# Kernel optimization log

Hardware: AMD Instinct MI355X
Metric: run time of the kernel (lower is better)

Reference implementation:

```python
import jax, jax.numpy as jnp
import numpy as np


def setup_inputs() -> dict:
    key = jax.random.key(0)
    ks = jax.random.split(key, 4)
    B, T, I, H, O = 1024, 512, 64, 128, 10
    return {
        "x": jax.random.normal(ks[0], (B, T, I), dtype=jnp.float32),
        "W_hx": jax.random.normal(ks[1], (H, I), dtype=jnp.float32) * (6.0 / (H + I)) ** 0.5,
        "W_hh": jax.random.normal(ks[2], (H, H), dtype=jnp.float32) * (6.0 / (H + H)) ** 0.5,
        "b_hh": jnp.zeros((H,), dtype=jnp.float32),
        "W_ph": jax.random.normal(ks[3], (O, H), dtype=jnp.float32) * (6.0 / (O + H)) ** 0.5,
        "b_ph": jnp.zeros((O,), dtype=jnp.float32),
    }


def reference(x, W_hx, W_hh, b_hh, W_ph, b_ph):
    B, T, I = x.shape
    H = W_hh.shape[0]
    # Precompute input projections for all timesteps in one GEMM: [B,T,H]
    xproj = jnp.einsum("bti,hi->bth", x, W_hx)
    h0 = jnp.zeros((B, H), dtype=x.dtype)

    def step(h, xp_t):
        # xp_t: [B,H]; recurrent update h = tanh(W_hx x_t + W_hh h + b)
        h_new = jnp.tanh(xp_t + h @ W_hh.T + b_hh)
        return h_new, None

    # scan over time (leading axis): xproj transposed to [T,B,H]
    h_T, _ = jax.lax.scan(step, h0, jnp.swapaxes(xproj, 0, 1))
    return h_T @ W_ph.T + b_ph
```

## Files before the change

### kernel.cpp

```cpp
#include <hip/hip_runtime.h>
#include <math.h>


#define T_STEPS 512
#define I_DIM   64
#define H_DIM   128
#define O_DIM   10
#define BT      16
#define PITCH   136

typedef short  bf16x8 __attribute__((ext_vector_type(8)));
typedef float  f32x4  __attribute__((ext_vector_type(4)));

static __device__ inline short f2bf(float f) {
    union { float f; unsigned u; } v; v.f = f;
    unsigned r = v.u + 0x7FFFu + ((v.u >> 16) & 1u);
    return (short)(r >> 16);
}
static __device__ inline float bf2f(short s) {
    union { unsigned u; float f; } v; v.u = ((unsigned)(unsigned short)s) << 16;
    return v.f;
}

__global__ __launch_bounds__(256)
__attribute__((amdgpu_waves_per_eu(1, 2)))
void rnn_mfma_kernel(
    const float* __restrict__ x,
    const float* __restrict__ W_hx,
    const float* __restrict__ W_hh,
    const float* __restrict__ b_hh,
    const float* __restrict__ W_ph,
    const float* __restrict__ b_ph,
    float* __restrict__ out)
{
    const int b0   = blockIdx.x * BT;
    const int tid  = threadIdx.x;
    const int w    = tid >> 6;
    const int lane = tid & 63;
    const int c    = lane & 15;
    const int q    = lane >> 4;

    __shared__ short hbuf[2][BT * PITCH];

    int4 Bw[2][6];
    #pragma unroll
    for (int nt = 0; nt < 2; ++nt) {
        const int n = w * 32 + nt * 16 + c;
        #pragma unroll
        for (int kt = 0; kt < 6; ++kt) {
            const float* src = (kt < 4) ? (W_hh + n * H_DIM + kt * 32 + q * 8)
                                        : (W_hx + n * I_DIM + (kt - 4) * 32 + q * 8);
            short e[8];
            #pragma unroll
            for (int j = 0; j < 8; ++j) e[j] = f2bf(src[j]);
            Bw[nt][kt].x = ((int)(unsigned short)e[0]) | ((int)(unsigned short)e[1] << 16);
            Bw[nt][kt].y = ((int)(unsigned short)e[2]) | ((int)(unsigned short)e[3] << 16);
            Bw[nt][kt].z = ((int)(unsigned short)e[4]) | ((int)(unsigned short)e[5] << 16);
            Bw[nt][kt].w = ((int)(unsigned short)e[6]) | ((int)(unsigned short)e[7] << 16);
        }
    }
    #pragma unroll
    for (int nt = 0; nt < 2; ++nt)
        #pragma unroll
        for (int kt = 0; kt < 6; ++kt)
            asm volatile("" : "+v"(Bw[nt][kt].x), "+v"(Bw[nt][kt].y),
                              "+v"(Bw[nt][kt].z), "+v"(Bw[nt][kt].w));

    const float bias0 = b_hh[w * 32 + c];
    const float bias1 = b_hh[w * 32 + 16 + c];

    for (int idx = tid; idx < BT * PITCH; idx += 256) hbuf[0][idx] = 0;

    const float* xrow = x + (size_t)(b0 + c) * T_STEPS * I_DIM;
    float4 xr[4];
    {
        const float* p0 = xrow + 0 * I_DIM;
        xr[0] = *(const float4*)(p0 +      q * 8);
        xr[1] = *(const float4*)(p0 +      q * 8 + 4);
        xr[2] = *(const float4*)(p0 + 32 + q * 8);
        xr[3] = *(const float4*)(p0 + 32 + q * 8 + 4);
    }
    __syncthreads();

    for (int t = 0; t < T_STEPS; ++t) {
        const int p = t & 1;

        bf16x8 Ax0, Ax1;
        Ax0[0]=f2bf(xr[0].x); Ax0[1]=f2bf(xr[0].y); Ax0[2]=f2bf(xr[0].z); Ax0[3]=f2bf(xr[0].w);
        Ax0[4]=f2bf(xr[1].x); Ax0[5]=f2bf(xr[1].y); Ax0[6]=f2bf(xr[1].z); Ax0[7]=f2bf(xr[1].w);
        Ax1[0]=f2bf(xr[2].x); Ax1[1]=f2bf(xr[2].y); Ax1[2]=f2bf(xr[2].z); Ax1[3]=f2bf(xr[2].w);
        Ax1[4]=f2bf(xr[3].x); Ax1[5]=f2bf(xr[3].y); Ax1[6]=f2bf(xr[3].z); Ax1[7]=f2bf(xr[3].w);

        {
            const int tn = (t < T_STEPS - 1) ? (t + 1) : (T_STEPS - 1);
            const float* pn = xrow + (size_t)tn * I_DIM;
            xr[0] = *(const float4*)(pn +      q * 8);
            xr[1] = *(const float4*)(pn +      q * 8 + 4);
            xr[2] = *(const float4*)(pn + 32 + q * 8);
            xr[3] = *(const float4*)(pn + 32 + q * 8 + 4);
        }

        const short* hb = hbuf[p] + c * PITCH + q * 8;
        bf16x8 Ah0 = *(const bf16x8*)(hb +  0);
        bf16x8 Ah1 = *(const bf16x8*)(hb + 32);
        bf16x8 Ah2 = *(const bf16x8*)(hb + 64);
        bf16x8 Ah3 = *(const bf16x8*)(hb + 96);

        f32x4 C0 = {0.f, 0.f, 0.f, 0.f};
        f32x4 C1 = {0.f, 0.f, 0.f, 0.f};
        C0 = __builtin_amdgcn_mfma_f32_16x16x32_bf16(Ax0, __builtin_bit_cast(bf16x8, Bw[0][4]), C0, 0, 0, 0);
        C1 = __builtin_amdgcn_mfma_f32_16x16x32_bf16(Ax0, __builtin_bit_cast(bf16x8, Bw[1][4]), C1, 0, 0, 0);
        C0 = __builtin_amdgcn_mfma_f32_16x16x32_bf16(Ax1, __builtin_bit_cast(bf16x8, Bw[0][5]), C0, 0, 0, 0);
        C1 = __builtin_amdgcn_mfma_f32_16x16x32_bf16(Ax1, __builtin_bit_cast(bf16x8, Bw[1][5]), C1, 0, 0, 0);
        C0 = __builtin_amdgcn_mfma_f32_16x16x32_bf16(Ah0, __builtin_bit_cast(bf16x8, Bw[0][0]), C0, 0, 0, 0);
        C1 = __builtin_amdgcn_mfma_f32_16x16x32_bf16(Ah0, __builtin_bit_cast(bf16x8, Bw[1][0]), C1, 0, 0, 0);
        C0 = __builtin_amdgcn_mfma_f32_16x16x32_bf16(Ah1, __builtin_bit_cast(bf16x8, Bw[0][1]), C0, 0, 0, 0);
        C1 = __builtin_amdgcn_mfma_f32_16x16x32_bf16(Ah1, __builtin_bit_cast(bf16x8, Bw[1][1]), C1, 0, 0, 0);
        C0 = __builtin_amdgcn_mfma_f32_16x16x32_bf16(Ah2, __builtin_bit_cast(bf16x8, Bw[0][2]), C0, 0, 0, 0);
        C1 = __builtin_amdgcn_mfma_f32_16x16x32_bf16(Ah2, __builtin_bit_cast(bf16x8, Bw[1][2]), C1, 0, 0, 0);
        C0 = __builtin_amdgcn_mfma_f32_16x16x32_bf16(Ah3, __builtin_bit_cast(bf16x8, Bw[0][3]), C0, 0, 0, 0);
        C1 = __builtin_amdgcn_mfma_f32_16x16x32_bf16(Ah3, __builtin_bit_cast(bf16x8, Bw[1][3]), C1, 0, 0, 0);

        short* hw = hbuf[1 - p];
        #pragma unroll
        for (int r = 0; r < 4; ++r) {
            const int m = q * 4 + r;
            float s0 = C0[r] + bias0;
            float s1 = C1[r] + bias1;
            float e0 = __builtin_amdgcn_exp2f(s0 * 2.885390081777926825f);
            float e1 = __builtin_amdgcn_exp2f(s1 * 2.885390081777926825f);
            float h0 = fmaf(-2.0f, __builtin_amdgcn_rcpf(e0 + 1.0f), 1.0f);
            float h1 = fmaf(-2.0f, __builtin_amdgcn_rcpf(e1 + 1.0f), 1.0f);
            hw[m * PITCH + w * 32 + c]      = f2bf(h0);
            hw[m * PITCH + w * 32 + 16 + c] = f2bf(h1);
        }
        __syncthreads();
    }

    if (tid < BT * O_DIM) {
        const int m = tid / O_DIM;
        const int o = tid % O_DIM;
        float acc = b_ph[o];
        #pragma unroll 4
        for (int k = 0; k < H_DIM; ++k)
            acc = fmaf(W_ph[o * H_DIM + k], bf2f(hbuf[0][m * PITCH + k]), acc);
        out[(size_t)(b0 + m) * O_DIM + o] = acc;
    }
}

extern "C" void kernel_launch(void* const* d_in, const int* in_sizes, int n_in,
                              void* d_out, int out_size, void* d_ws, size_t ws_size,
                              hipStream_t stream) {
    const float* x    = (const float*)d_in[0];
    const float* W_hx = (const float*)d_in[1];
    const float* W_hh = (const float*)d_in[2];
    const float* b_hh = (const float*)d_in[3];
    const float* W_ph = (const float*)d_in[4];
    const float* b_ph = (const float*)d_in[5];
    float* out = (float*)d_out;

    rnn_mfma_kernel<<<1024 / BT, 256, 0, stream>>>(x, W_hx, W_hh, b_hh, W_ph, b_ph, out);
}
```

Measured before the change: 555.0 us.

## Unroll RNN loop by two with split accumulators and deeper x prefetch

Unrolls the time loop by two, alternating two x register buffers so x loads are prefetched two steps ahead instead of one. Each output tile is accumulated in two independent accumulator chains that are summed afterwards, which shortens the serial MFMA dependency chain. The hidden-state LDS reads now come before the x conversion, and __syncthreads is replaced with an explicit lgkmcnt wait plus s_barrier. The extra register buffers raise register pressure, and the added vector sums cost a few instructions per step.

Result: faster. 522.6 us (-5.8%).

```diff
diff --git a/kernel.cpp b/kernel.cpp
--- a/kernel.cpp
+++ b/kernel.cpp
@@ -21,6 +21,68 @@
     union { unsigned u; float f; } v; v.u = ((unsigned)(unsigned short)s) << 16;
     return v.f;
 }
+
+static __device__ inline void lds_barrier() {
+    asm volatile("s_waitcnt lgkmcnt(0)\n\ts_barrier" ::: "memory");
+}
+
+#define RNN_STEP(t, XR)                                                         \
+    {                                                                           \
+        const int p = (t) & 1;                                                  \
+         \
+        const short* hb = hbuf[p] + c * PITCH + q * 8;                          \
+        bf16x8 Ah0 = *(const bf16x8*)(hb +  0);                                 \
+        bf16x8 Ah1 = *(const bf16x8*)(hb + 32);                                 \
+        bf16x8 Ah2 = *(const bf16x8*)(hb + 64);                                 \
+        bf16x8 Ah3 = *(const bf16x8*)(hb + 96);                                 \
+          \
+          \
+        bf16x8 Ax0, Ax1;                                                        \
+        Ax0[0]=f2bf(XR[0].x); Ax0[1]=f2bf(XR[0].y); Ax0[2]=f2bf(XR[0].z); Ax0[3]=f2bf(XR[0].w); \
+        Ax0[4]=f2bf(XR[1].x); Ax0[5]=f2bf(XR[1].y); Ax0[6]=f2bf(XR[1].z); Ax0[7]=f2bf(XR[1].w); \
+        Ax1[0]=f2bf(XR[2].x); Ax1[1]=f2bf(XR[2].y); Ax1[2]=f2bf(XR[2].z); Ax1[3]=f2bf(XR[2].w); \
+        Ax1[4]=f2bf(XR[3].x); Ax1[5]=f2bf(XR[3].y); Ax1[6]=f2bf(XR[3].z); Ax1[7]=f2bf(XR[3].w); \
+        {                                                                       \
+            const int tn = ((t) + 2 < T_STEPS) ? (t) + 2 : T_STEPS - 1;         \
+            const float* pn = xrow + (size_t)tn * I_DIM;                        \
+            XR[0] = *(const float4*)(pn +      q * 8);                          \
+            XR[1] = *(const float4*)(pn +      q * 8 + 4);                      \
+            XR[2] = *(const float4*)(pn + 32 + q * 8);                          \
+            XR[3] = *(const float4*)(pn + 32 + q * 8 + 4);                      \
+        }                                                                       \
+            \
+        f32x4 C0a = {0.f,0.f,0.f,0.f}, C0b = {0.f,0.f,0.f,0.f};                 \
+        f32x4 C1a = {0.f,0.f,0.f,0.f}, C1b = {0.f,0.f,0.f,0.f};                 \
+        C0a = __builtin_amdgcn_mfma_f32_16x16x32_bf16(Ax0, __builtin_bit_cast(bf16x8, Bw[0][4]), C0a, 0, 0, 0); \
+        C1a = __builtin_amdgcn_mfma_f32_16x16x32_bf16(Ax0, __builtin_bit_cast(bf16x8, Bw[1][4]), C1a, 0, 0, 0); \
+        C0b = __builtin_amdgcn_mfma_f32_16x16x32_bf16(Ax1, __builtin_bit_cast(bf16x8, Bw[0][5]), C0b, 0, 0, 0); \
+        C1b = __builtin_amdgcn_mfma_f32_16x16x32_bf16(Ax1, __builtin_bit_cast(bf16x8, Bw[1][5]), C1b, 0, 0, 0); \
+        C0a = __builtin_amdgcn_mfma_f32_16x16x32_bf16(Ah0, __builtin_bit_cast(bf16x8, Bw[0][0]), C0a, 0, 0, 0); \
+        C1a = __builtin_amdgcn_mfma_f32_16x16x32_bf16(Ah0, __builtin_bit_cast(bf16x8, Bw[1][0]), C1a, 0, 0, 0); \
+        C0b = __builtin_amdgcn_mfma_f32_16x16x32_bf16(Ah1, __builtin_bit_cast(bf16x8, Bw[0][1]), C0b, 0, 0, 0); \
+        C1b = __builtin_amdgcn_mfma_f32_16x16x32_bf16(Ah1, __builtin_bit_cast(bf16x8, Bw[1][1]), C1b, 0, 0, 0); \
+        C0a = __builtin_amdgcn_mfma_f32_16x16x32_bf16(Ah2, __builtin_bit_cast(bf16x8, Bw[0][2]), C0a, 0, 0, 0); \
+        C1a = __builtin_amdgcn_mfma_f32_16x16x32_bf16(Ah2, __builtin_bit_cast(bf16x8, Bw[1][2]), C1a, 0, 0, 0); \
+        C0b = __builtin_amdgcn_mfma_f32_16x16x32_bf16(Ah3, __builtin_bit_cast(bf16x8, Bw[0][3]), C0b, 0, 0, 0); \
+        C1b = __builtin_amdgcn_mfma_f32_16x16x32_bf16(Ah3, __builtin_bit_cast(bf16x8, Bw[1][3]), C1b, 0, 0, 0); \
+        const f32x4 C0 = C0a + C0b;                                             \
+        const f32x4 C1 = C1a + C1b;                                             \
+              \
+        short* hw = hbuf[1 - p];                                                \
+        _Pragma("unroll")                                                       \
+        for (int r = 0; r < 4; ++r) {                                           \
+            const int m = q * 4 + r;                                            \
+            float s0 = C0[r] + bias0;                                           \
+            float s1 = C1[r] + bias1;                                           \
+            float e0 = __builtin_amdgcn_exp2f(s0 * 2.885390081777926825f);      \
+            float e1 = __builtin_amdgcn_exp2f(s1 * 2.885390081777926825f);      \
+            float h0 = fmaf(-2.0f, __builtin_amdgcn_rcpf(e0 + 1.0f), 1.0f);     \
+            float h1 = fmaf(-2.0f, __builtin_amdgcn_rcpf(e1 + 1.0f), 1.0f);     \
+            hw[m * PITCH + w * 32 + c]      = f2bf(h0);                         \
+            hw[m * PITCH + w * 32 + 16 + c] = f2bf(h1);                         \
+        }                                                                       \
+        lds_barrier();               \
+    }
 
 __global__ __launch_bounds__(256)
 __attribute__((amdgpu_waves_per_eu(1, 2)))
@@ -72,69 +134,25 @@
     for (int idx = tid; idx < BT * PITCH; idx += 256) hbuf[0][idx] = 0;
 
     const float* xrow = x + (size_t)(b0 + c) * T_STEPS * I_DIM;
-    float4 xr[4];
+    float4 xrA[4], xrB[4];
     {
-        const float* p0 = xrow + 0 * I_DIM;
-        xr[0] = *(const float4*)(p0 +      q * 8);
-        xr[1] = *(const float4*)(p0 +      q * 8 + 4);
-        xr[2] = *(const float4*)(p0 + 32 + q * 8);
-        xr[3] = *(const float4*)(p0 + 32 + q * 8 + 4);
+        const float* p0 = xrow;
+        xrA[0] = *(const float4*)(p0 +      q * 8);
+        xrA[1] = *(const float4*)(p0 +      q * 8 + 4);
+        xrA[2] = *(const float4*)(p0 + 32 + q * 8);
+        xrA[3] = *(const float4*)(p0 + 32 + q * 8 + 4);
+        const float* p1 = xrow + I_DIM;
+        xrB[0] = *(const float4*)(p1 +      q * 8);
+        xrB[1] = *(const float4*)(p1 +      q * 8 + 4);
+        xrB[2] = *(const float4*)(p1 + 32 + q * 8);
+        xrB[3] = *(const float4*)(p1 + 32 + q * 8 + 4);
     }
     __syncthreads();
 
-    for (int t = 0; t < T_STEPS; ++t) {
-        const int p = t & 1;
-
-        bf16x8 Ax0, Ax1;
-        Ax0[0]=f2bf(xr[0].x); Ax0[1]=f2bf(xr[0].y); Ax0[2]=f2bf(xr[0].z); Ax0[3]=f2bf(xr[0].w);
-        Ax0[4]=f2bf(xr[1].x); Ax0[5]=f2bf(xr[1].y); Ax0[6]=f2bf(xr[1].z); Ax0[7]=f2bf(xr[1].w);
-        Ax1[0]=f2bf(xr[2].x); Ax1[1]=f2bf(xr[2].y); Ax1[2]=f2bf(xr[2].z); Ax1[3]=f2bf(xr[2].w);
-        Ax1[4]=f2bf(xr[3].x); Ax1[5]=f2bf(xr[3].y); Ax1[6]=f2bf(xr[3].z); Ax1[7]=f2bf(xr[3].w);
-
-        {
-            const int tn = (t < T_STEPS - 1) ? (t + 1) : (T_STEPS - 1);
-            const float* pn = xrow + (size_t)tn * I_DIM;
-            xr[0] = *(const float4*)(pn +      q * 8);
-            xr[1] = *(const float4*)(pn +      q * 8 + 4);
-            xr[2] = *(const float4*)(pn + 32 + q * 8);
-            xr[3] = *(const float4*)(pn + 32 + q * 8 + 4);
-        }
-
-        const short* hb = hbuf[p] + c * PITCH + q * 8;
-        bf16x8 Ah0 = *(const bf16x8*)(hb +  0);
-        bf16x8 Ah1 = *(const bf16x8*)(hb + 32);
-        bf16x8 Ah2 = *(const bf16x8*)(hb + 64);
-        bf16x8 Ah3 = *(const bf16x8*)(hb + 96);
-
-        f32x4 C0 = {0.f, 0.f, 0.f, 0.f};
-        f32x4 C1 = {0.f, 0.f, 0.f, 0.f};
-        C0 = __builtin_amdgcn_mfma_f32_16x16x32_bf16(Ax0, __builtin_bit_cast(bf16x8, Bw[0][4]), C0, 0, 0, 0);
-        C1 = __builtin_amdgcn_mfma_f32_16x16x32_bf16(Ax0, __builtin_bit_cast(bf16x8, Bw[1][4]), C1, 0, 0, 0);
-        C0 = __builtin_amdgcn_mfma_f32_16x16x32_bf16(Ax1, __builtin_bit_cast(bf16x8, Bw[0][5]), C0, 0, 0, 0);
-        C1 = __builtin_amdgcn_mfma_f32_16x16x32_bf16(Ax1, __builtin_bit_cast(bf16x8, Bw[1][5]), C1, 0, 0, 0);
-        C0 = __builtin_amdgcn_mfma_f32_16x16x32_bf16(Ah0, __builtin_bit_cast(bf16x8, Bw[0][0]), C0, 0, 0, 0);
-        C1 = __builtin_amdgcn_mfma_f32_16x16x32_bf16(Ah0, __builtin_bit_cast(bf16x8, Bw[1][0]), C1, 0, 0, 0);
-        C0 = __builtin_amdgcn_mfma_f32_16x16x32_bf16(Ah1, __builtin_bit_cast(bf16x8, Bw[0][1]), C0, 0, 0, 0);
-        C1 = __builtin_amdgcn_mfma_f32_16x16x32_bf16(Ah1, __builtin_bit_cast(bf16x8, Bw[1][1]), C1, 0, 0, 0);
-        C0 = __builtin_amdgcn_mfma_f32_16x16x32_bf16(Ah2, __builtin_bit_cast(bf16x8, Bw[0][2]), C0, 0, 0, 0);
-        C1 = __builtin_amdgcn_mfma_f32_16x16x32_bf16(Ah2, __builtin_bit_cast(bf16x8, Bw[1][2]), C1, 0, 0, 0);
-        C0 = __builtin_amdgcn_mfma_f32_16x16x32_bf16(Ah3, __builtin_bit_cast(bf16x8, Bw[0][3]), C0, 0, 0, 0);
-        C1 = __builtin_amdgcn_mfma_f32_16x16x32_bf16(Ah3, __builtin_bit_cast(bf16x8, Bw[1][3]), C1, 0, 0, 0);
-
-        short* hw = hbuf[1 - p];
-        #pragma unroll
-        for (int r = 0; r < 4; ++r) {
-            const int m = q * 4 + r;
-            float s0 = C0[r] + bias0;
-            float s1 = C1[r] + bias1;
-            float e0 = __builtin_amdgcn_exp2f(s0 * 2.885390081777926825f);
-            float e1 = __builtin_amdgcn_exp2f(s1 * 2.885390081777926825f);
-            float h0 = fmaf(-2.0f, __builtin_amdgcn_rcpf(e0 + 1.0f), 1.0f);
-            float h1 = fmaf(-2.0f, __builtin_amdgcn_rcpf(e1 + 1.0f), 1.0f);
-            hw[m * PITCH + w * 32 + c]      = f2bf(h0);
-            hw[m * PITCH + w * 32 + 16 + c] = f2bf(h1);
-        }
-        __syncthreads();
+    #pragma unroll 1
+    for (int t = 0; t < T_STEPS; t += 2) {
+        RNN_STEP(t,     xrA)
+        RNN_STEP(t + 1, xrB)
     }
 
     if (tid < BT * O_DIM) {
```
